# Kernel tuning notes

Hardware: AMD Instinct MI355X
Metric: run time of the kernel (lower is better)

## Reference

```python
import jax, jax.numpy as jnp
import numpy as np

D = 768       # GATv2 in/out feats (num_heads=1)
D_OUT = 384   # fc output
K = 51        # round(top_rate * L) = round(0.1 * 512)
EPS = 1e-5    # nn.LayerNorm default eps


def _layer_norm(x, g, b):
    mu = jnp.mean(x, axis=-1, keepdims=True)
    var = jnp.mean((x - mu) ** 2, axis=-1, keepdims=True)
    return (x - mu) / jnp.sqrt(var + EPS) * g + b


def setup_inputs() -> dict:
    key = jax.random.key(0)
    ks = jax.random.split(key, 12)
    B, L = 4, 512
    s = 0.02
    return {
        "hidden_state": jax.random.normal(ks[0], (B, L, D), jnp.float32),
        "attention": jax.random.uniform(ks[1], (B, L, L), jnp.float32),
        # GATv2Conv params (fc_src, fc_dst, attn vector, output bias)
        "W_src": jax.random.normal(ks[2], (D, D), jnp.float32) * s,
        "b_src": jnp.zeros((D,), jnp.float32),
        "W_dst": jax.random.normal(ks[3], (D, D), jnp.float32) * s,
        "b_dst": jnp.zeros((D,), jnp.float32),
        "attn_vec": jax.random.normal(ks[4], (D,), jnp.float32) * s,
        "gat_bias": jnp.zeros((D,), jnp.float32),
        # GlobalAttentionPooling gate_nn: Linear(768, 1)
        "gate_W": jax.random.normal(ks[5], (D, 1), jnp.float32) * s,
        "gate_b": jnp.zeros((1,), jnp.float32),
        # LayerNorm(768)
        "ln_g": jnp.ones((D,), jnp.float32),
        "ln_b": jnp.zeros((D,), jnp.float32),
        # fc: Linear(768, 384)
        "fc_W": jax.random.normal(ks[6], (D, D_OUT), jnp.float32) * s,
        "fc_b": jnp.zeros((D_OUT,), jnp.float32),
        # LayerNorm(384)
        "ln2_g": jnp.ones((D_OUT,), jnp.float32),
        "ln2_b": jnp.zeros((D_OUT,), jnp.float32),
        "mask": jnp.ones((B, L), jnp.int32),  # unused by the original forward
        "type": 0,                              # unused string/type flag
    }


def reference(hidden_state, attention, W_src, b_src, W_dst, b_dst, attn_vec,
              gat_bias, gate_W, gate_b, ln_g, ln_b, fc_W, fc_b, ln2_g, ln2_b,
              mask, type):
    B, L, _ = hidden_state.shape
    # --- topk sparsification: each node i keeps K source neighbors ---
    vals, idx = jax.lax.top_k(attention, K)          # [B, L, K]
    valid = vals > 0.0                                # edges kept by pos_sign filter

    # --- GATv2Conv (num_heads=1, residual=Identity since 768==768) ---
    feat_src = hidden_state @ W_src + b_src           # [B, L, D]
    feat_dst = hidden_state @ W_dst + b_dst           # [B, L, D]
    g = feat_src[jnp.arange(B)[:, None, None], idx]   # [B, L, K, D] gathered src feats
    e = jax.nn.leaky_relu(g + feat_dst[:, :, None, :], 0.2)
    scores = jnp.einsum("blkd,d->blk", e, attn_vec)   # [B, L, K]
    scores = jnp.where(valid, scores, -1e9)           # removed edges masked out
    a = jax.nn.softmax(scores, axis=-1)               # edge_softmax per dst node
    h = jnp.einsum("blk,blkd->bld", a, g)             # weighted scatter-sum
    h = h + hidden_state + gat_bias                   # residual (identity) + bias
    h = jax.nn.leaky_relu(h, 0.01)                    # nn.LeakyReLU activation

    # --- GlobalAttentionPooling: softmax(gate) weighted segment reduce ---
    gate = h @ gate_W + gate_b                        # [B, L, 1]
    p = jax.nn.softmax(gate, axis=1)
    pooled = jnp.sum(p * h, axis=1)                   # [B, D]

    # --- head: fc(dropout(ln(relu(out)))) then ln2 (dropout = eval identity) ---
    out = _layer_norm(jax.nn.relu(pooled), ln_g, ln_b)
    out = out @ fc_W + fc_b
    out = _layer_norm(out, ln2_g, ln2_b)
    return out
```

## Files before the change

### kernel.cpp

```cpp
#include <hip/hip_runtime.h>
#include <math.h>

#define D 768
#define DOUT 384
#define LSEQ 512
#define BATCH 4
#define KTOP 51
#define EPS 1e-5f

typedef unsigned short ushort_t;
typedef __bf16 bf16x8 __attribute__((ext_vector_type(8)));
typedef float f32x4 __attribute__((ext_vector_type(4)));
typedef float f32x2 __attribute__((ext_vector_type(2)));

#define GLOAD16(gp, lp)                                                        \
    __builtin_amdgcn_global_load_lds(                                          \
        (const __attribute__((address_space(1))) unsigned int*)(gp),           \
        (__attribute__((address_space(3))) unsigned int*)(lp), 16, 0, 0)

__device__ __forceinline__ ushort_t f2bf(float f) {
    unsigned int u = __builtin_bit_cast(unsigned int, f);
    u = (u + 0x7FFFu + ((u >> 16) & 1u)) >> 16;
    return (ushort_t)u;
}

__device__ __forceinline__ float bf2f(ushort_t u) {
    unsigned int v = ((unsigned int)u) << 16;
    return __builtin_bit_cast(float, v);
}

__global__ __launch_bounds__(256) void prep_kernel(const float* __restrict__ hidden,
                                                   ushort_t* __restrict__ Ah,
                                                   const float* __restrict__ W0,
                                                   const float* __restrict__ W1,
                                                   ushort_t* __restrict__ WT0,
                                                   ushort_t* __restrict__ WT1,
                                                   float* __restrict__ pooled,
                                                   float* __restrict__ z,
                                                   const float* __restrict__ attn,
                                                   int* __restrict__ kidg,
                                                   float* __restrict__ kvvg) {
    __shared__ float tile[32][33];
    __shared__ float vals[LSEQ];
    __shared__ float cval[320];
    __shared__ int   cidx[320];
    __shared__ int   nhi, outSlot;
    __shared__ int   kid[KTOP];
    __shared__ float kvv[KTOP];

    const int bid = blockIdx.x;
    const int tid = threadIdx.x;
    if (bid < 1536) {
        const int i = (bid * 256 + tid) * 4;
        const float4 v = *(const float4*)(hidden + i);
        ushort4 o;
        o.x = f2bf(v.x); o.y = f2bf(v.y); o.z = f2bf(v.z); o.w = f2bf(v.w);
        *(ushort4*)(Ah + i) = o;
    } else if (bid < 2688) {
        const int t = bid - 1536;
        const int zz = t / 576;
        const int rem = t - zz * 576;
        const int by = rem / 24, bx = rem - by * 24;
        const float* W = zz ? W1 : W0;
        ushort_t* WT = zz ? WT1 : WT0;
        const int kbase = by * 32;
        const int nbase = bx * 32;
        const int r = tid >> 3, c4 = (tid & 7) * 4;

        const float4 v = *(const float4*)(W + (size_t)(kbase + r) * D + nbase + c4);
        tile[r][c4 + 0] = v.x; tile[r][c4 + 1] = v.y;
        tile[r][c4 + 2] = v.z; tile[r][c4 + 3] = v.w;
        __syncthreads();
        ushort4 o;
        o.x = f2bf(tile[c4 + 0][r]); o.y = f2bf(tile[c4 + 1][r]);
        o.z = f2bf(tile[c4 + 2][r]); o.w = f2bf(tile[c4 + 3][r]);
        *(ushort4*)(WT + (size_t)(nbase + r) * D + kbase + c4) = o;
    } else if (bid == 2688) {
        for (int i = tid; i < BATCH * D; i += 256) pooled[i] = 0.f;
        for (int i = tid; i < BATCH * DOUT; i += 256) z[i] = 0.f;
    } else {
        const int row = bid - 2689;
        const int lane = tid & 63;
        if (tid == 0) { nhi = 0; outSlot = 0; }

        const float* a = attn + (size_t)row * LSEQ;
        const float v0 = a[tid];
        const float v1 = a[tid + 256];
        vals[tid] = v0;
        vals[tid + 256] = v1;
        __syncthreads();

        {
            const unsigned long long m0 = __ballot(v0 > 0.75f);
            const unsigned long long m1 = __ballot(v1 > 0.75f);
            const int c0 = __popcll(m0);
            const int c1 = __popcll(m1);
            int base = 0;
            if (lane == 0) base = atomicAdd(&nhi, c0 + c1);
            base = __shfl(base, 0);
            const unsigned long long below = (1ull << lane) - 1ull;
            if (v0 > 0.75f) {
                const int s = base + __popcll(m0 & below);
                if (s < 320) { cval[s] = v0; cidx[s] = tid; }
            }
            if (v1 > 0.75f) {
                const int s = base + c0 + __popcll(m1 & below);
                if (s < 320) { cval[s] = v1; cidx[s] = tid + 256; }
            }
        }
        __syncthreads();

        const int n = nhi;
        if (n >= KTOP && n <= 320) {
            if (tid < n) {
                const float v = cval[tid];
                const int e = cidx[tid];
                int r = 0;
                int j = 0;
                const int n4 = n & ~3;
                for (; j < n4; j += 4) {
                    const float4 u4 = *(const float4*)&cval[j];
                    const int4 e4 = *(const int4*)&cidx[j];
                    r += (u4.x > v) || (u4.x == v && e4.x < e);
                    r += (u4.y > v) || (u4.y == v && e4.y < e);
                    r += (u4.z > v) || (u4.z == v && e4.z < e);
                    r += (u4.w > v) || (u4.w == v && e4.w < e);
                }
                for (; j < n; ++j) {
                    const float u = cval[j];
                    r += (u > v) || (u == v && cidx[j] < e);
                }
                const bool keep = (r < KTOP);
                const unsigned long long mk = __ballot(keep);
                const int cnt = __popcll(mk);
                if (cnt > 0) {
                    const int leader = __ffsll((unsigned long long)mk) - 1;
                    int base = 0;
                    if (lane == leader) base = atomicAdd(&outSlot, cnt);
                    base = __shfl(base, leader);
                    if (keep) {
                        const int s = base + __popcll(mk & ((1ull << lane) - 1ull));
                        kid[s] = e; kvv[s] = v;
                    }
                }
            }
        } else {
#pragma unroll
            for (int e0 = 0; e0 < 2; ++e0) {
                const int e = tid + e0 * 256;
                const float v = vals[e];
                int r = 0;
                for (int j = 0; j < LSEQ; ++j) {
                    const float u = vals[j];
                    r += (u > v) || (u == v && j < e);
                }
                if (r < KTOP) {
                    const int s = atomicAdd(&outSlot, 1);
                    kid[s] = e; kvv[s] = v;
                }
            }
        }
        __syncthreads();
        if (tid < KTOP) {
            kidg[(size_t)row * 64 + tid] = kid[tid];
            kvvg[(size_t)row * 64 + tid] = kvv[tid];
        }
    }
}

__global__ __launch_bounds__(256) void feat_gemm_kernel(const ushort_t* __restrict__ Ah,
                                                        const ushort_t* __restrict__ WT0,
                                                        const float* __restrict__ b0,
                                                        ushort_t* __restrict__ Csrc_bf,
                                                        const ushort_t* __restrict__ WT1,
                                                        const float* __restrict__ b1,
                                                        float* __restrict__ Cdst) {
    const int bid = blockIdx.x;
    const int wid = (bid & 7) * 96 + (bid >> 3);
    const int zz = wid / 384;
    const int rem = wid - zz * 384;
    const int tileY = rem / 12;
    const int tileX = rem - tileY * 12;

    const ushort_t* WT = zz ? WT1 : WT0;
    const float* bias = zz ? b1 : b0;

    __shared__ ushort_t As[64 * 64];
    __shared__ ushort_t Bs[64 * 64];

    const int tid = threadIdx.x;
    const int lane = tid & 63;
    const int wave = tid >> 6;
    const int quad = lane >> 4;
    const int m15 = lane & 15;
    const int qRow = (wave & 1) * 32;
    const int qCol = (wave >> 1) * 32;

    const int rowBase = tileY * 64;
    const int colBase = tileX * 64;

    const int e0 = tid * 8;
    const int r0 = e0 >> 6;
    const int c0 = e0 & 63;
    const int cc = c0 >> 3;
    const int csw = (cc ^ (r0 & 7)) << 3;
    const ushort_t* Abase = Ah + (size_t)rowBase * D;
    const ushort_t* Bbase = WT + (size_t)colBase * D;

    f32x4 acc[2][2] = {};

    for (int kk = 0; kk < D; kk += 64) {
        __syncthreads();
        GLOAD16(Abase + (size_t)r0 * D + kk + csw, &As[e0]);
        GLOAD16(Abase + (size_t)(r0 + 32) * D + kk + csw, &As[e0 + 2048]);
        GLOAD16(Bbase + (size_t)r0 * D + kk + csw, &Bs[e0]);
        GLOAD16(Bbase + (size_t)(r0 + 32) * D + kk + csw, &Bs[e0 + 2048]);
        __syncthreads();

        bf16x8 a[2][2], b[2][2];
#pragma unroll
        for (int i = 0; i < 2; ++i) {
            const int row = qRow + i * 16 + m15;
            const int sw = row & 7;
#pragma unroll
            for (int ks = 0; ks < 2; ++ks)
                a[i][ks] = *(const bf16x8*)&As[row * 64 + ((((ks << 2) + quad) ^ sw) << 3)];
        }
#pragma unroll
        for (int j = 0; j < 2; ++j) {
            const int row = qCol + j * 16 + m15;
            const int sw = row & 7;
#pragma unroll
            for (int ks = 0; ks < 2; ++ks)
                b[j][ks] = *(const bf16x8*)&Bs[row * 64 + ((((ks << 2) + quad) ^ sw) << 3)];
        }
#pragma unroll
        for (int ks = 0; ks < 2; ++ks)
#pragma unroll
            for (int i = 0; i < 2; ++i)
#pragma unroll
                for (int j = 0; j < 2; ++j)
                    acc[i][j] = __builtin_amdgcn_mfma_f32_16x16x32_bf16(a[i][ks], b[j][ks], acc[i][j], 0, 0, 0);
    }

    if (zz == 0) {
#pragma unroll
        for (int j = 0; j < 2; ++j) {
            const int col = colBase + qCol + j * 16 + m15;
            const float bv = bias[col];
#pragma unroll
            for (int i = 0; i < 2; ++i) {
                ushort_t* Cp = Csrc_bf + (size_t)(rowBase + qRow + i * 16 + quad * 4) * D + col;
#pragma unroll
                for (int r = 0; r < 4; ++r)
                    Cp[(size_t)r * D] = f2bf(acc[i][j][r] + bv);
            }
        }
    } else {
#pragma unroll
        for (int j = 0; j < 2; ++j) {
            const int col = colBase + qCol + j * 16 + m15;
            const float bv = bias[col];
#pragma unroll
            for (int i = 0; i < 2; ++i) {
                float* Cp = Cdst + (size_t)(rowBase + qRow + i * 16 + quad * 4) * D + col;
#pragma unroll
                for (int r = 0; r < 4; ++r)
                    Cp[(size_t)r * D] = acc[i][j][r] + bv;
            }
        }
    }
}

__global__ __launch_bounds__(256) void scoregath_kernel(const int* __restrict__ kidg,
                                                        const float* __restrict__ kvvg,
                                                        const ushort_t* __restrict__ fsrc_bf,
                                                        const float* __restrict__ feat_dst,
                                                        const float* __restrict__ attn_vec,
                                                        const float* __restrict__ gat_bias,
                                                        const float* __restrict__ hidden,
                                                        const float* __restrict__ gate_W,
                                                        const float* __restrict__ gate_b,
                                                        ushort_t* __restrict__ h,
                                                        float* __restrict__ gate) {
    const int bid = blockIdx.x;
    const int row = (bid & 7) * 256 + (bid >> 3);
    const int b = row >> 9;
    const int tid = threadIdx.x;
    const int lane = tid & 63;
    const int wave = tid >> 6;

    __shared__ int   kid[KTOP];
    __shared__ float kvv[KTOP];
    __shared__ float wm[4], wl[4];
    __shared__ float hpart[4][D];
    __shared__ float gred[4];

    if (tid < KTOP) {
        kid[tid] = kidg[(size_t)row * 64 + tid];
        kvv[tid] = kvvg[(size_t)row * 64 + tid];
    }

    const int d0 = lane * 8;
    const int d1 = 512 + lane * 4;
    const float* fdp = feat_dst + (size_t)row * D;
    f32x2 fdr[6], avr[6];
    {
        const float4 f0 = *(const float4*)(fdp + d0);
        const float4 f1 = *(const float4*)(fdp + d0 + 4);
        const float4 f2 = *(const float4*)(fdp + d1);
        const float4 a0 = *(const float4*)(attn_vec + d0);
        const float4 a1 = *(const float4*)(attn_vec + d0 + 4);
        const float4 a2 = *(const float4*)(attn_vec + d1);
        fdr[0] = f32x2{f0.x, f0.y}; fdr[1] = f32x2{f0.z, f0.w};
        fdr[2] = f32x2{f1.x, f1.y}; fdr[3] = f32x2{f1.z, f1.w};
        fdr[4] = f32x2{f2.x, f2.y}; fdr[5] = f32x2{f2.z, f2.w};
        avr[0] = f32x2{a0.x, a0.y}; avr[1] = f32x2{a0.z, a0.w};
        avr[2] = f32x2{a1.x, a1.y}; avr[3] = f32x2{a1.z, a1.w};
        avr[4] = f32x2{a2.x, a2.y}; avr[5] = f32x2{a2.z, a2.w};
    }
    __syncthreads();

    const ushort_t* fb = fsrc_bf + ((size_t)(b << 9)) * D;
    float m_run = -3.0e38f, l_run = 0.f;
    f32x2 acc[6] = {};

    const ushort_t* gp0 = fb + (size_t)kid[wave] * D;
    bf16x8 cg0 = *(const bf16x8*)(gp0 + d0);
    ushort4 cg1 = *(const ushort4*)(gp0 + d1);

    for (int k = wave; k < KTOP; k += 4) {
        const int kn = (k + 4 < KTOP) ? (k + 4) : k;
        const ushort_t* gn = fb + (size_t)kid[kn] * D;
        const bf16x8 ng0 = *(const bf16x8*)(gn + d0);
        const ushort4 ng1 = *(const ushort4*)(gn + d1);

        f32x2 gf[6];
        gf[0] = f32x2{(float)cg0[0], (float)cg0[1]};
        gf[1] = f32x2{(float)cg0[2], (float)cg0[3]};
        gf[2] = f32x2{(float)cg0[4], (float)cg0[5]};
        gf[3] = f32x2{(float)cg0[6], (float)cg0[7]};
        gf[4] = f32x2{bf2f(cg1.x), bf2f(cg1.y)};
        gf[5] = f32x2{bf2f(cg1.z), bf2f(cg1.w)};

        f32x2 s2 = {0.f, 0.f};
#pragma unroll
        for (int jj = 0; jj < 6; ++jj) {
            f32x2 x = gf[jj] + fdr[jj];
            x = __builtin_elementwise_max(x, x * 0.2f);
            s2 += x * avr[jj];
        }
        float s = s2.x + s2.y;
#pragma unroll
        for (int off = 32; off > 0; off >>= 1) s += __shfl_xor(s, off);
        s = (kvv[k] > 0.f) ? s : -1e9f;

        if (s > m_run + 8.f) {
            const float rs = __expf(m_run - s);
            l_run *= rs;
#pragma unroll
            for (int jj = 0; jj < 6; ++jj) acc[jj] *= rs;
            m_run = s;
        }
        const float p = __expf(s - m_run);
        l_run += p;
#pragma unroll
        for (int jj = 0; jj < 6; ++jj) acc[jj] += p * gf[jj];

        cg0 = ng0; cg1 = ng1;
    }

    if (lane == 0) { wm[wave] = m_run; wl[wave] = l_run; }
    *(f32x2*)&hpart[wave][d0]     = acc[0];
    *(f32x2*)&hpart[wave][d0 + 2] = acc[1];
    *(f32x2*)&hpart[wave][d0 + 4] = acc[2];
    *(f32x2*)&hpart[wave][d0 + 6] = acc[3];
    *(f32x2*)&hpart[wave][d1]     = acc[4];
    *(f32x2*)&hpart[wave][d1 + 2] = acc[5];
    __syncthreads();

    const float M = fmaxf(fmaxf(wm[0], wm[1]), fmaxf(wm[2], wm[3]));
    const float r0 = __expf(wm[0] - M), r1 = __expf(wm[1] - M);
    const float r2 = __expf(wm[2] - M), r3 = __expf(wm[3] - M);
    const float invL = 1.f / (r0 * wl[0] + r1 * wl[1] + r2 * wl[2] + r3 * wl[3]);

    float dotp = 0.f;
    const float* hid = hidden + (size_t)row * D;
    ushort_t* hb = h + (size_t)row * D;
#pragma unroll
    for (int j = 0; j < 3; ++j) {
        const int d = tid + j * 256;
        const float hv = (r0 * hpart[0][d] + r1 * hpart[1][d] +
                          r2 * hpart[2][d] + r3 * hpart[3][d]) * invL;
        float v = hv + hid[d] + gat_bias[d];
        v = v > 0.f ? v : 0.01f * v;
        hb[d] = f2bf(v);
        dotp += v * gate_W[d];
    }
#pragma unroll
    for (int off = 32; off > 0; off >>= 1) dotp += __shfl_xor(dotp, off);
    if (lane == 0) gred[wave] = dotp;
    __syncthreads();
    if (tid == 0) gate[row] = gate_b[0] + gred[0] + gred[1] + gred[2] + gred[3];
}

__global__ __launch_bounds__(256) void pool_kernel(const ushort_t* __restrict__ h,
                                                   const float* __restrict__ gate,
                                                   float* __restrict__ pooled) {
    const int b = blockIdx.z;
    const int lbase = blockIdx.y * 64;
    const int d = blockIdx.x * 256 + threadIdx.x;
    const int tid = threadIdx.x;
    const int lane = tid & 63;
    const int w = tid >> 6;

    __shared__ float wred[4];
    __shared__ float ps[64];

    const float g0 = gate[b * LSEQ + tid];
    const float g1 = gate[b * LSEQ + tid + 256];
    float m = fmaxf(g0, g1);
#pragma unroll
    for (int off = 32; off > 0; off >>= 1) m = fmaxf(m, __shfl_xor(m, off));
    if (lane == 0) wred[w] = m;
    __syncthreads();
    m = fmaxf(fmaxf(wred[0], wred[1]), fmaxf(wred[2], wred[3]));
    float e = __expf(g0 - m) + __expf(g1 - m);
#pragma unroll
    for (int off = 32; off > 0; off >>= 1) e += __shfl_xor(e, off);
    __syncthreads();
    if (lane == 0) wred[w] = e;
    __syncthreads();
    const float inv = 1.f / (wred[0] + wred[1] + wred[2] + wred[3]);
    if (tid < 64) ps[tid] = __expf(gate[b * LSEQ + lbase + tid] - m) * inv;
    __syncthreads();

    const ushort_t* hb = h + ((size_t)(b * LSEQ + lbase)) * D + d;
    float acc = 0.f;
#pragma unroll 8
    for (int l = 0; l < 64; ++l) {
        acc += ps[l] * bf2f(hb[(size_t)l * D]);
    }
    atomicAdd(&pooled[b * D + d], acc);
}

__global__ __launch_bounds__(256) void fc_kernel(const float* __restrict__ pooled,
                                                 const float* __restrict__ ln_g,
                                                 const float* __restrict__ ln_b,
                                                 const float* __restrict__ fc_W,
                                                 float* __restrict__ z) {
    const int b = blockIdx.z;
    const int by = blockIdx.y;
    const int dbase = by * 256;
    const int jbase = blockIdx.x * 64;
    const int tid = threadIdx.x;
    const int lane = tid & 63;
    const int w = tid >> 6;
    const int jt = tid & 63;
    const int sub = tid >> 6;

    __shared__ float wred[4];
    __shared__ float ys[256];
    __shared__ float part[4][64];

    float v[3];
#pragma unroll
    for (int i = 0; i < 3; ++i) v[i] = fmaxf(pooled[b * D + tid + i * 256], 0.f);

    float s = v[0] + v[1] + v[2];
#pragma unroll
    for (int off = 32; off > 0; off >>= 1) s += __shfl_xor(s, off);
    if (lane == 0) wred[w] = s;
    __syncthreads();
    const float mu = (wred[0] + wred[1] + wred[2] + wred[3]) / (float)D;
    float vs = 0.f;
#pragma unroll
    for (int i = 0; i < 3; ++i) { const float dd = v[i] - mu; vs += dd * dd; }
#pragma unroll
    for (int off = 32; off > 0; off >>= 1) vs += __shfl_xor(vs, off);
    __syncthreads();
    if (lane == 0) wred[w] = vs;
    __syncthreads();
    const float rstd = rsqrtf((wred[0] + wred[1] + wred[2] + wred[3]) / (float)D + EPS);

    const float vb = (by == 0) ? v[0] : (by == 1 ? v[1] : v[2]);
    ys[tid] = (vb - mu) * rstd * ln_g[dbase + tid] + ln_b[dbase + tid];
    __syncthreads();

    const float* W = fc_W + (size_t)(dbase + sub * 64) * DOUT + jbase + jt;
    const float* yy = ys + sub * 64;
    float acc = 0.f;
#pragma unroll 8
    for (int i = 0; i < 64; ++i) {
        acc += yy[i] * W[(size_t)i * DOUT];
    }
    part[sub][jt] = acc;
    __syncthreads();
    if (sub == 0) {
        const float tot = part[0][jt] + part[1][jt] + part[2][jt] + part[3][jt];
        atomicAdd(&z[b * DOUT + jbase + jt], tot);
    }
}

__global__ __launch_bounds__(384) void ln2_kernel(const float* __restrict__ z,
                                                  const float* __restrict__ fc_b,
                                                  const float* __restrict__ ln2_g,
                                                  const float* __restrict__ ln2_b,
                                                  float* __restrict__ out) {
    const int b = blockIdx.x;
    const int tid = threadIdx.x;
    const int lane = tid & 63;
    const int wave = tid >> 6;
    __shared__ float wred[6];

    const float v = z[b * DOUT + tid] + fc_b[tid];

    float s = v;
#pragma unroll
    for (int off = 32; off > 0; off >>= 1) s += __shfl_xor(s, off);
    if (lane == 0) wred[wave] = s;
    __syncthreads();
    float mu = 0.f;
#pragma unroll
    for (int w = 0; w < 6; ++w) mu += wred[w];
    mu /= (float)DOUT;
    __syncthreads();

    const float dd = v - mu;
    float s2 = dd * dd;
#pragma unroll
    for (int off = 32; off > 0; off >>= 1) s2 += __shfl_xor(s2, off);
    if (lane == 0) wred[wave] = s2;
    __syncthreads();
    float var = 0.f;
#pragma unroll
    for (int w = 0; w < 6; ++w) var += wred[w];
    const float rstd = rsqrtf(var / (float)DOUT + EPS);

    out[b * DOUT + tid] = dd * rstd * ln2_g[tid] + ln2_b[tid];
}

extern "C" void kernel_launch(void* const* d_in, const int* in_sizes, int n_in,
                              void* d_out, int out_size, void* d_ws, size_t ws_size,
                              hipStream_t stream) {
    const float* hidden   = (const float*)d_in[0];
    const float* attention= (const float*)d_in[1];
    const float* W_src    = (const float*)d_in[2];
    const float* b_src    = (const float*)d_in[3];
    const float* W_dst    = (const float*)d_in[4];
    const float* b_dst    = (const float*)d_in[5];
    const float* attn_vec = (const float*)d_in[6];
    const float* gat_bias = (const float*)d_in[7];
    const float* gate_W   = (const float*)d_in[8];
    const float* gate_b   = (const float*)d_in[9];
    const float* ln_g     = (const float*)d_in[10];
    const float* ln_b     = (const float*)d_in[11];
    const float* fc_W     = (const float*)d_in[12];
    const float* fc_b     = (const float*)d_in[13];
    const float* ln2_g    = (const float*)d_in[14];
    const float* ln2_b    = (const float*)d_in[15];
    float* out = (float*)d_out;

    const int M = BATCH * LSEQ;
    float* feat_dst = (float*)d_ws;
    float* gate     = feat_dst + (size_t)M * D;
    float* pooled   = gate + M;
    float* z        = pooled + BATCH * D;
    float* kvvg     = z + BATCH * DOUT;
    int*   kidg     = (int*)(kvvg + (size_t)M * 64);
    ushort_t* Ah    = (ushort_t*)(kidg + (size_t)M * 64);
    ushort_t* WT0   = Ah + (size_t)M * D;
    ushort_t* WT1   = WT0 + (size_t)D * D;
    ushort_t* fsrcb = WT1 + (size_t)D * D;
    ushort_t* h     = fsrcb + (size_t)M * D;

    hipLaunchKernelGGL(prep_kernel, dim3(2689 + M), dim3(256), 0, stream,
                       hidden, Ah, W_src, W_dst, WT0, WT1, pooled, z,
                       attention, kidg, kvvg);
    hipLaunchKernelGGL(feat_gemm_kernel, dim3(768), dim3(256), 0, stream,
                       Ah, WT0, b_src, fsrcb, WT1, b_dst, feat_dst);
    hipLaunchKernelGGL(scoregath_kernel, dim3(M), dim3(256), 0, stream,
                       kidg, kvvg, fsrcb, feat_dst, attn_vec, gat_bias, hidden,
                       gate_W, gate_b, h, gate);
    hipLaunchKernelGGL(pool_kernel, dim3(D / 256, LSEQ / 64, BATCH), dim3(256), 0, stream,
                       h, gate, pooled);
    hipLaunchKernelGGL(fc_kernel, dim3(DOUT / 64, D / 256, BATCH), dim3(256), 0, stream,
                       pooled, ln_g, ln_b, fc_W, z);
    hipLaunchKernelGGL(ln2_kernel, dim3(BATCH), dim3(384), 0, stream,
                       z, fc_b, ln2_g, ln2_b, out);
}
```

Baseline: 147.7 us.

## Widen score-gather blocks to eight waves and fuse final LayerNorm into fc

The score/gather kernel now runs 512 threads (8 waves) per destination row, so each wave handles fewer of the 51 neighbors and the partial softmax and accumulator merge covers 8 partials. The separate ln2 kernel is removed: fc blocks bump a per-batch counter after their atomic z updates, and the last block of each batch applies bias plus LayerNorm. This removes one launch and adds more parallelism per row, at the cost of larger shared memory, more merge work and a threadfence/counter protocol.

```diff
diff --git a/kernel.cpp b/kernel.cpp
--- a/kernel.cpp
+++ b/kernel.cpp
@@ -37,6 +37,7 @@
                                                    ushort_t* __restrict__ WT1,
                                                    float* __restrict__ pooled,
                                                    float* __restrict__ z,
+                                                   int* __restrict__ cnt,
                                                    const float* __restrict__ attn,
                                                    int* __restrict__ kidg,
                                                    float* __restrict__ kvvg) {
@@ -78,6 +79,7 @@
     } else if (bid == 2688) {
         for (int i = tid; i < BATCH * D; i += 256) pooled[i] = 0.f;
         for (int i = tid; i < BATCH * DOUT; i += 256) z[i] = 0.f;
+        if (tid < BATCH) cnt[tid] = 0;
     } else {
         const int row = bid - 2689;
         const int lane = tid & 63;
@@ -132,11 +134,11 @@
                 }
                 const bool keep = (r < KTOP);
                 const unsigned long long mk = __ballot(keep);
-                const int cnt = __popcll(mk);
-                if (cnt > 0) {
+                const int cntk = __popcll(mk);
+                if (cntk > 0) {
                     const int leader = __ffsll((unsigned long long)mk) - 1;
                     int base = 0;
-                    if (lane == leader) base = atomicAdd(&outSlot, cnt);
+                    if (lane == leader) base = atomicAdd(&outSlot, cntk);
                     base = __shfl(base, leader);
                     if (keep) {
                         const int s = base + __popcll(mk & ((1ull << lane) - 1ull));
@@ -272,7 +274,7 @@
     }
 }
 
-__global__ __launch_bounds__(256) void scoregath_kernel(const int* __restrict__ kidg,
+__global__ __launch_bounds__(512) void scoregath_kernel(const int* __restrict__ kidg,
                                                         const float* __restrict__ kvvg,
                                                         const ushort_t* __restrict__ fsrc_bf,
                                                         const float* __restrict__ feat_dst,
@@ -292,9 +294,9 @@
 
     __shared__ int   kid[KTOP];
     __shared__ float kvv[KTOP];
-    __shared__ float wm[4], wl[4];
-    __shared__ float hpart[4][D];
-    __shared__ float gred[4];
+    __shared__ float wm[8], wl[8];
+    __shared__ float hpart[8][D];
+    __shared__ float gred[8];
 
     if (tid < KTOP) {
         kid[tid] = kidg[(size_t)row * 64 + tid];
@@ -329,8 +331,8 @@
     bf16x8 cg0 = *(const bf16x8*)(gp0 + d0);
     ushort4 cg1 = *(const ushort4*)(gp0 + d1);
 
-    for (int k = wave; k < KTOP; k += 4) {
-        const int kn = (k + 4 < KTOP) ? (k + 4) : k;
+    for (int k = wave; k < KTOP; k += 8) {
+        const int kn = (k + 8 < KTOP) ? (k + 8) : k;
         const ushort_t* gn = fb + (size_t)kid[kn] * D;
         const bf16x8 ng0 = *(const bf16x8*)(gn + d0);
         const ushort4 ng1 = *(const ushort4*)(gn + d1);
@@ -379,29 +381,50 @@
     *(f32x2*)&hpart[wave][d1 + 2] = acc[5];
     __syncthreads();
 
-    const float M = fmaxf(fmaxf(wm[0], wm[1]), fmaxf(wm[2], wm[3]));
-    const float r0 = __expf(wm[0] - M), r1 = __expf(wm[1] - M);
-    const float r2 = __expf(wm[2] - M), r3 = __expf(wm[3] - M);
-    const float invL = 1.f / (r0 * wl[0] + r1 * wl[1] + r2 * wl[2] + r3 * wl[3]);
+    float M = wm[0];
+#pragma unroll
+    for (int w = 1; w < 8; ++w) M = fmaxf(M, wm[w]);
+    float rw[8];
+    float Lsum = 0.f;
+#pragma unroll
+    for (int w = 0; w < 8; ++w) { rw[w] = __expf(wm[w] - M); Lsum += rw[w] * wl[w]; }
+    const float invL = 1.f / Lsum;
 
     float dotp = 0.f;
     const float* hid = hidden + (size_t)row * D;
     ushort_t* hb = h + (size_t)row * D;
-#pragma unroll
-    for (int j = 0; j < 3; ++j) {
-        const int d = tid + j * 256;
-        const float hv = (r0 * hpart[0][d] + r1 * hpart[1][d] +
-                          r2 * hpart[2][d] + r3 * hpart[3][d]) * invL;
+    {
+        const int d = tid;
+        float hv = 0.f;
+#pragma unroll
+        for (int w = 0; w < 8; ++w) hv += rw[w] * hpart[w][d];
+        hv *= invL;
         float v = hv + hid[d] + gat_bias[d];
         v = v > 0.f ? v : 0.01f * v;
         hb[d] = f2bf(v);
         dotp += v * gate_W[d];
     }
+    if (tid < 256) {
+        const int d = tid + 512;
+        float hv = 0.f;
+#pragma unroll
+        for (int w = 0; w < 8; ++w) hv += rw[w] * hpart[w][d];
+        hv *= invL;
+        float v = hv + hid[d] + gat_bias[d];
+        v = v > 0.f ? v : 0.01f * v;
+        hb[d] = f2bf(v);
+        dotp += v * gate_W[d];
+    }
 #pragma unroll
     for (int off = 32; off > 0; off >>= 1) dotp += __shfl_xor(dotp, off);
     if (lane == 0) gred[wave] = dotp;
     __syncthreads();
-    if (tid == 0) gate[row] = gate_b[0] + gred[0] + gred[1] + gred[2] + gred[3];
+    if (tid == 0) {
+        float g = gate_b[0];
+#pragma unroll
+        for (int w = 0; w < 8; ++w) g += gred[w];
+        gate[row] = g;
+    }
 }
 
 __global__ __launch_bounds__(256) void pool_kernel(const ushort_t* __restrict__ h,
@@ -448,7 +471,12 @@
                                                  const float* __restrict__ ln_g,
                                                  const float* __restrict__ ln_b,
                                                  const float* __restrict__ fc_W,
-                                                 float* __restrict__ z) {
+                                                 float* __restrict__ z,
+                                                 int* __restrict__ cnt,
+                                                 const float* __restrict__ fc_b,
+                                                 const float* __restrict__ ln2_g,
+                                                 const float* __restrict__ ln2_b,
+                                                 float* __restrict__ out) {
     const int b = blockIdx.z;
     const int by = blockIdx.y;
     const int dbase = by * 256;
@@ -462,6 +490,7 @@
     __shared__ float wred[4];
     __shared__ float ys[256];
     __shared__ float part[4][64];
+    __shared__ int   amLast;
 
     float v[3];
 #pragma unroll
@@ -500,44 +529,39 @@
         const float tot = part[0][jt] + part[1][jt] + part[2][jt] + part[3][jt];
         atomicAdd(&z[b * DOUT + jbase + jt], tot);
     }
-}
-
-__global__ __launch_bounds__(384) void ln2_kernel(const float* __restrict__ z,
-                                                  const float* __restrict__ fc_b,
-                                                  const float* __restrict__ ln2_g,
-                                                  const float* __restrict__ ln2_b,
-                                                  float* __restrict__ out) {
-    const int b = blockIdx.x;
-    const int tid = threadIdx.x;
-    const int lane = tid & 63;
-    const int wave = tid >> 6;
-    __shared__ float wred[6];
-
-    const float v = z[b * DOUT + tid] + fc_b[tid];
-
-    float s = v;
-#pragma unroll
-    for (int off = 32; off > 0; off >>= 1) s += __shfl_xor(s, off);
-    if (lane == 0) wred[wave] = s;
-    __syncthreads();
-    float mu = 0.f;
-#pragma unroll
-    for (int w = 0; w < 6; ++w) mu += wred[w];
-    mu /= (float)DOUT;
-    __syncthreads();
-
-    const float dd = v - mu;
-    float s2 = dd * dd;
+
+    __threadfence();
+    __syncthreads();
+    if (tid == 0) amLast = (atomicAdd(&cnt[b], 1) == 17);
+    __syncthreads();
+    if (!amLast) return;
+    __threadfence();
+
+    const bool has2 = tid < (DOUT - 256);
+    const float v0 = z[b * DOUT + tid] + fc_b[tid];
+    const float v1 = has2 ? z[b * DOUT + tid + 256] + fc_b[tid + 256] : 0.f;
+
+    float sm = v0 + v1;
+#pragma unroll
+    for (int off = 32; off > 0; off >>= 1) sm += __shfl_xor(sm, off);
+    __syncthreads();
+    if (lane == 0) wred[w] = sm;
+    __syncthreads();
+    const float mu2 = (wred[0] + wred[1] + wred[2] + wred[3]) / (float)DOUT;
+
+    const float dd0 = v0 - mu2;
+    const float dd1 = v1 - mu2;
+    float s2 = dd0 * dd0 + (has2 ? dd1 * dd1 : 0.f);
 #pragma unroll
     for (int off = 32; off > 0; off >>= 1) s2 += __shfl_xor(s2, off);
-    if (lane == 0) wred[wave] = s2;
-    __syncthreads();
-    float var = 0.f;
-#pragma unroll
-    for (int w = 0; w < 6; ++w) var += wred[w];
-    const float rstd = rsqrtf(var / (float)DOUT + EPS);
-
-    out[b * DOUT + tid] = dd * rstd * ln2_g[tid] + ln2_b[tid];
+    __syncthreads();
+    if (lane == 0) wred[w] = s2;
+    __syncthreads();
+    const float rstd2 = rsqrtf((wred[0] + wred[1] + wred[2] + wred[3]) / (float)DOUT + EPS);
+
+    out[b * DOUT + tid] = dd0 * rstd2 * ln2_g[tid] + ln2_b[tid];
+    if (has2)
+        out[b * DOUT + tid + 256] = dd1 * rstd2 * ln2_g[tid + 256] + ln2_b[tid + 256];
 }
 
 extern "C" void kernel_launch(void* const* d_in, const int* in_sizes, int n_in,
@@ -566,7 +590,8 @@
     float* gate     = feat_dst + (size_t)M * D;
     float* pooled   = gate + M;
     float* z        = pooled + BATCH * D;
-    float* kvvg     = z + BATCH * DOUT;
+    int*   cnt      = (int*)(z + BATCH * DOUT);
+    float* kvvg     = (float*)(cnt + 64);
     int*   kidg     = (int*)(kvvg + (size_t)M * 64);
     ushort_t* Ah    = (ushort_t*)(kidg + (size_t)M * 64);
     ushort_t* WT0   = Ah + (size_t)M * D;
@@ -575,17 +600,15 @@
     ushort_t* h     = fsrcb + (size_t)M * D;
 
     hipLaunchKernelGGL(prep_kernel, dim3(2689 + M), dim3(256), 0, stream,
-                       hidden, Ah, W_src, W_dst, WT0, WT1, pooled, z,
+                       hidden, Ah, W_src, W_dst, WT0, WT1, pooled, z, cnt,
                        attention, kidg, kvvg);
     hipLaunchKernelGGL(feat_gemm_kernel, dim3(768), dim3(256), 0, stream,
                        Ah, WT0, b_src, fsrcb, WT1, b_dst, feat_dst);
-    hipLaunchKernelGGL(scoregath_kernel, dim3(M), dim3(256), 0, stream,
+    hipLaunchKernelGGL(scoregath_kernel, dim3(M), dim3(512), 0, stream,
                        kidg, kvvg, fsrcb, feat_dst, attn_vec, gat_bias, hidden,
                        gate_W, gate_b, h, gate);
     hipLaunchKernelGGL(pool_kernel, dim3(D / 256, LSEQ / 64, BATCH), dim3(256), 0, stream,
                        h, gate, pooled);
     hipLaunchKernelGGL(fc_kernel, dim3(DOUT / 64, D / 256, BATCH), dim3(256), 0, stream,
-                       pooled, ln_g, ln_b, fc_W, z);
-    hipLaunchKernelGGL(ln2_kernel, dim3(BATCH), dim3(384), 0, stream,
-                       z, fc_b, ln2_g, ln2_b, out);
-}
+                       pooled, ln_g, ln_b, fc_W, z, cnt, fc_b, ln2_g, ln2_b, out);
+}
```

New measurement: 158.6 us. +7.3%, slower.
